# Kernel optimization log

Measured on AMD Instinct MI355X. Metric: run time of the kernel, lower is better.

## Reference

```python
import jax, jax.numpy as jnp
import numpy as np

ODIM = 8192      # output dim (slice target)
MSIZE = 64       # tile size
N_BLOCKS = 1024  # size of shared block bank


def setup_inputs() -> dict:
    key = jax.random.key(0)
    k1, k2, k3, k4 = jax.random.split(key, 4)
    x = jax.random.normal(k1, (256, 8192), dtype=jnp.float32)
    # bank of msize x msize module blocks (scaled like fan-in init)
    blocks = jax.random.normal(k2, (N_BLOCKS, MSIZE, MSIZE), dtype=jnp.float32) * 0.02
    bound = 1.0 / np.sqrt(ODIM).astype(np.float32)
    bias = jax.random.uniform(k3, (ODIM,), dtype=jnp.float32, minval=-bound, maxval=bound)
    # parts: [icount, ocount] indices into the block bank
    parts = jax.random.randint(k4, (128, 128), 0, N_BLOCKS)
    return {"x": x, "blocks": blocks, "bias": bias, "parts": parts}


def reference(x, blocks, bias, parts):
    icount, ocount = parts.shape
    m = blocks.shape[-1]
    # build_mosaic: gather blocks per parts and tile into a dense weight matrix
    fc = blocks[parts]                                   # [ic, oc, m, m]
    fc_mat = fc.transpose(0, 2, 1, 3).reshape(icount * m, ocount * m)
    # idim (8192) is divisible by msize, so pad is identity (rem == 0 branch)
    y = x @ fc_mat                                       # [B, oc*m]
    y = y[..., :ODIM] + bias                             # slice + bias; post = Identity
    return y
```

## Files before the change

### kernel.cpp

```cpp
#include <hip/hip_runtime.h>
#include <stdint.h>

#define BATCH 256
#define IDIM  8192
#define ODIM  8192
#define MS    64
#define IC    128
#define OC    128
#define NB    1024

#define TM 128
#define TN 128
#define KSPLIT 4
#define NIB (IC / KSPLIT)

#define A_BASE(s) ((s) * 8192)
#define B_BASE(s) (16384 + (s) * 8192)

typedef __bf16 bf16x8 __attribute__((ext_vector_type(8)));
typedef float  floatx4 __attribute__((ext_vector_type(4)));

#define WAITCNT_VM(n) ((((n) & 15) | (((n) >> 4) << 14)) | 0x70 | 0xF00)

__device__ __forceinline__ void async_load16(unsigned short* lds_p, const unsigned short* g_p) {
    __builtin_amdgcn_global_load_lds(
        (const __attribute__((address_space(1))) unsigned int*)g_p,
        (__attribute__((address_space(3))) unsigned int*)lds_p,
        16, 0, 0);
}

__device__ __forceinline__ unsigned short f32_to_bf16(float f) {
    unsigned int u = __float_as_uint(f);
    u += 0x7FFFu + ((u >> 16) & 1u);
    return (unsigned short)(u >> 16);
}

#define XCONV_BLKS 1024
#define PT_BLKS 64
__global__ void k_convert(const float* __restrict__ x, const float* __restrict__ blocks,
                          const int* __restrict__ parts,
                          unsigned short* __restrict__ xb, unsigned short* __restrict__ bt,
                          int* __restrict__ pT) {
    __shared__ float tile[MS][MS + 1];
    int b = blockIdx.x;
    if (b < NB) {
        const float4* src4 = (const float4*)(blocks + (size_t)b * MS * MS);
        unsigned short* dst = bt + (size_t)b * MS * MS;
        #pragma unroll
        for (int i = 0; i < 4; ++i) {
            int slot = i * 256 + threadIdx.x;
            int r = slot >> 4, c4 = (slot & 15) * 4;
            float4 v = src4[slot];
            tile[r][c4 + 0] = v.x; tile[r][c4 + 1] = v.y;
            tile[r][c4 + 2] = v.z; tile[r][c4 + 3] = v.w;
        }
        __syncthreads();
        #pragma unroll
        for (int i = 0; i < 2; ++i) {
            int slot = i * 256 + threadIdx.x;
            int c = slot >> 3, o = slot & 7;
            union { unsigned short s[8]; uint4 v; } u;
            #pragma unroll
            for (int j = 0; j < 8; ++j) u.s[j] = f32_to_bf16(tile[o * 8 + j][c]);
            *(uint4*)(dst + c * MS + o * 8) = u.v;
        }
    } else if (b < NB + XCONV_BLKS) {
        int t = (b - NB) * 256 + threadIdx.x;
        const float4* x4 = (const float4*)x;
        float4 a = x4[2 * t], bb = x4[2 * t + 1];
        union { unsigned short s[8]; uint4 v; } u;
        u.s[0] = f32_to_bf16(a.x);  u.s[1] = f32_to_bf16(a.y);
        u.s[2] = f32_to_bf16(a.z);  u.s[3] = f32_to_bf16(a.w);
        u.s[4] = f32_to_bf16(bb.x); u.s[5] = f32_to_bf16(bb.y);
        u.s[6] = f32_to_bf16(bb.z); u.s[7] = f32_to_bf16(bb.w);
        ((uint4*)xb)[t] = u.v;
    } else {
        int t = (b - NB - XCONV_BLKS) * 256 + threadIdx.x;
        int oc = t >> 7, ic = t & 127;
        pT[t] = parts[ic * OC + oc];
    }
}

extern __shared__ unsigned short smem[];

__global__ __launch_bounds__(256, 2)
void k_mosaic_gemm(const unsigned short* __restrict__ xb,
                   const unsigned short* __restrict__ bt,
                   const int* __restrict__ pT,
                   float* __restrict__ partial) {
    const int tid  = threadIdx.x;
    const int lane = tid & 63;
    const int wave = tid >> 6;
    const int wrow = wave >> 1;
    const int wcol = wave & 1;
    const int nt = blockIdx.x;
    const int mt = blockIdx.y;
    const int ks = blockIdx.z;

    const int m0  = mt * TM;
    const int ob0 = nt * 2;
    const int ib0 = ks * NIB;

    const int row  = lane & 15;
    const int quad = lane >> 4;

    int pv0 = pT[ob0 * IC + ib0 + (lane & 31)];
    int pv1 = pT[(ob0 + 1) * IC + ib0 + (lane & 31)];

    int a_off[2][4], b_off[2][4];
    #pragma unroll
    for (int kk = 0; kk < 2; ++kk) {
        int oct = kk * 4 + quad;
        #pragma unroll
        for (int mi = 0; mi < 4; ++mi) {
            int r = wrow * 64 + mi * 16 + row;
            a_off[kk][mi] = r * MS + ((oct ^ (r & 7)) << 3);
        }
        #pragma unroll
        for (int ni = 0; ni < 4; ++ni) {
            int n = wcol * 64 + ni * 16 + row;
            b_off[kk][ni] = n * MS + ((oct ^ (n & 7)) << 3);
        }
    }

    floatx4 acc[4][4];
    #pragma unroll
    for (int mi = 0; mi < 4; ++mi)
        #pragma unroll
        for (int ni = 0; ni < 4; ++ni)
            acc[mi][ni] = (floatx4){0.f, 0.f, 0.f, 0.f};

#define STAGE_A(abase, ibx) do {                                              \
    _Pragma("unroll")                                                         \
    for (int j = 0; j < 4; ++j) {                                             \
        int slot = j * 256 + tid;               \
        int m = slot >> 3;                                                    \
        int oct = (slot & 7) ^ (m & 7);                                       \
        async_load16(smem + (abase) + slot * 8,                               \
                     xb + (size_t)(m0 + m) * IDIM + (ibx) * MS + oct * 8);    \
    } } while (0)

#define STAGE_B(bbase, pa, pb) do {                                           \
    _Pragma("unroll")                                                         \
    for (int j = 0; j < 4; ++j) {                                             \
        int slot = j * 256 + tid;               \
        int n = slot >> 3;                                                    \
        int oct = (slot & 7) ^ (n & 7);                                       \
        int p = (j < 2) ? (pa) : (pb);                                        \
        async_load16(smem + (bbase) + slot * 8,                               \
                     bt + (size_t)p * (MS * MS) + (n & 63) * MS + oct * 8);   \
    } } while (0)

#define COMPUTE(abase, bbase) do {                                            \
    _Pragma("unroll")                                                         \
    for (int kk = 0; kk < 2; ++kk) {                                          \
        bf16x8 af[4], bfr[4];                                                 \
        _Pragma("unroll")                                                     \
        for (int mi = 0; mi < 4; ++mi)                                        \
            af[mi] = *(const bf16x8*)(smem + (abase) + a_off[kk][mi]);        \
        _Pragma("unroll")                                                     \
        for (int ni = 0; ni < 4; ++ni)                                        \
            bfr[ni] = *(const bf16x8*)(smem + (bbase) + b_off[kk][ni]);       \
        _Pragma("unroll")                                                     \
        for (int mi = 0; mi < 4; ++mi)                                        \
            _Pragma("unroll")                                                 \
            for (int ni = 0; ni < 4; ++ni)                                    \
                acc[mi][ni] = __builtin_amdgcn_mfma_f32_16x16x32_bf16(        \
                    af[mi], bfr[ni], acc[mi][ni], 0, 0, 0);                   \
    } } while (0)

#define ROUND(idx, acS, bcS, asS, bsS) do {                                   \
    STAGE_A(A_BASE(asS), ib0 + (idx) + 1);                                    \
    { int q0 = __shfl(pv0, (idx) + 2), q1 = __shfl(pv1, (idx) + 2);           \
      STAGE_B(B_BASE(bsS), q0, q1); }                                         \
    __builtin_amdgcn_sched_barrier(0);                                        \
    __builtin_amdgcn_s_waitcnt(WAITCNT_VM(12));                               \
    __builtin_amdgcn_s_barrier();                                             \
    __builtin_amdgcn_sched_barrier(0);                                        \
    COMPUTE(A_BASE(acS), B_BASE(bcS));                                        \
    __builtin_amdgcn_sched_barrier(0);                                        \
    __builtin_amdgcn_s_barrier();                                             \
    __builtin_amdgcn_sched_barrier(0);                                        \
    } while (0)

    STAGE_A(A_BASE(0), ib0 + 0);
    { int q0 = __shfl(pv0, 0), q1 = __shfl(pv1, 0); STAGE_B(B_BASE(0), q0, q1); }
    { int q0 = __shfl(pv0, 1), q1 = __shfl(pv1, 1); STAGE_B(B_BASE(1), q0, q1); }

    for (int i6 = 0; i6 < 30; i6 += 6) {
        ROUND(i6 + 0, 0, 0, 1, 2);
        ROUND(i6 + 1, 1, 1, 0, 0);
        ROUND(i6 + 2, 0, 2, 1, 1);
        ROUND(i6 + 3, 1, 0, 0, 2);
        ROUND(i6 + 4, 0, 1, 1, 0);
        ROUND(i6 + 5, 1, 2, 0, 1);
    }
    STAGE_A(A_BASE(1), ib0 + NIB - 1);
    __builtin_amdgcn_sched_barrier(0);
    __builtin_amdgcn_s_waitcnt(WAITCNT_VM(8));
    __builtin_amdgcn_s_barrier();
    __builtin_amdgcn_sched_barrier(0);
    COMPUTE(A_BASE(0), B_BASE(0));
    __builtin_amdgcn_sched_barrier(0);
    __builtin_amdgcn_s_barrier();
    __builtin_amdgcn_sched_barrier(0);
    __builtin_amdgcn_s_waitcnt(WAITCNT_VM(0));
    __builtin_amdgcn_s_barrier();
    __builtin_amdgcn_sched_barrier(0);
    COMPUTE(A_BASE(1), B_BASE(1));

    float* out = partial + (size_t)ks * BATCH * ODIM;
    #pragma unroll
    for (int mi = 0; mi < 4; ++mi)
        #pragma unroll
        for (int ni = 0; ni < 4; ++ni)
            #pragma unroll
            for (int r = 0; r < 4; ++r) {
                int rowg = m0 + wrow * 64 + mi * 16 + quad * 4 + r;
                int colg = nt * TN + wcol * 64 + ni * 16 + row;
                out[(size_t)rowg * ODIM + colg] = acc[mi][ni][r];
            }
}

__global__ void k_reduce_bias(const float* __restrict__ partial,
                              const float* __restrict__ bias,
                              float* __restrict__ out) {
    int t = blockIdx.x * 256 + threadIdx.x;
    const float4* b4 = (const float4*)bias;
    float4 c = b4[t & (ODIM / 4 - 1)];
    float4 r = {c.x, c.y, c.z, c.w};
    #pragma unroll
    for (int k = 0; k < KSPLIT; ++k) {
        const float4* p = (const float4*)(partial + (size_t)k * BATCH * ODIM);
        float4 a = p[t];
        r.x += a.x; r.y += a.y; r.z += a.z; r.w += a.w;
    }
    ((float4*)out)[t] = r;
}

extern "C" void kernel_launch(void* const* d_in, const int* in_sizes, int n_in,
                              void* d_out, int out_size, void* d_ws, size_t ws_size,
                              hipStream_t stream) {
    const float* x      = (const float*)d_in[0];
    const float* blocks = (const float*)d_in[1];
    const float* bias   = (const float*)d_in[2];
    const int*   parts  = (const int*)d_in[3];
    float* out = (float*)d_out;

    char* ws = (char*)d_ws;
    unsigned short* xb      = (unsigned short*)ws;
    unsigned short* btb     = (unsigned short*)(ws + (4u << 20));
    int*            pTr     = (int*)(ws + (12u << 20));
    float*          partial = (float*)(ws + (13u << 20));

    static bool attr_set = false;
    if (!attr_set) {
        hipFuncSetAttribute((const void*)k_mosaic_gemm,
                            hipFuncAttributeMaxDynamicSharedMemorySize, 80 * 1024);
        attr_set = true;
    }

    k_convert<<<NB + XCONV_BLKS + PT_BLKS, 256, 0, stream>>>(x, blocks, parts, xb, btb, pTr);
    k_mosaic_gemm<<<dim3(ODIM / TN, BATCH / TM, KSPLIT), 256, 80 * 1024, stream>>>(xb, btb, pTr, partial);
    k_reduce_bias<<<(BATCH * ODIM) / (256 * 4), 256, 0, stream>>>(partial, bias, out);
}
```

Before: 121.4 us.

## Switch GEMM to 256x256 tiles with 512 threads and 8-way K split

Replaces the 128x128-tile, 4-way split-K mosaic GEMM with 256x256 tiles computed by 512-thread blocks over an 8-way K split. The 64-wide K step is double-buffered, with loads and MFMAs interleaved in quarter-tile phases and raised wave priority around the MFMA bursts. The goal is more data reuse per LDS byte and a full one-block-per-CU grid of 256 blocks. In exchange it doubles the split-K partial buffer, so the reduce kernel's memory traffic grows. It also needs 128 KB of LDS, which leaves one block per CU.

Measured after the change: 127.8 us. 1.05x slower.

```diff
diff --git a/kernel.cpp b/kernel.cpp
--- a/kernel.cpp
+++ b/kernel.cpp
@@ -9,13 +9,14 @@
 #define OC    128
 #define NB    1024
 
-#define TM 128
-#define TN 128
-#define KSPLIT 4
-#define NIB (IC / KSPLIT)
-
-#define A_BASE(s) ((s) * 8192)
-#define B_BASE(s) (16384 + (s) * 8192)
+#define BM 256
+#define BN 256
+#define BK 64
+#define KSPLIT 8
+#define KT (IC / KSPLIT)
+
+#define ABUF(s) ((s) * 16384)
+#define BBUF(s) (32768 + (s) * 16384)
 
 typedef __bf16 bf16x8 __attribute__((ext_vector_type(8)));
 typedef float  floatx4 __attribute__((ext_vector_type(4)));
@@ -83,7 +84,7 @@
 
 extern __shared__ unsigned short smem[];
 
-__global__ __launch_bounds__(256, 2)
+__global__ __launch_bounds__(512, 2)
 void k_mosaic_gemm(const unsigned short* __restrict__ xb,
                    const unsigned short* __restrict__ bt,
                    const int* __restrict__ pT,
@@ -91,134 +92,136 @@
     const int tid  = threadIdx.x;
     const int lane = tid & 63;
     const int wave = tid >> 6;
-    const int wrow = wave >> 1;
-    const int wcol = wave & 1;
-    const int nt = blockIdx.x;
-    const int mt = blockIdx.y;
-    const int ks = blockIdx.z;
-
-    const int m0  = mt * TM;
-    const int ob0 = nt * 2;
-    const int ib0 = ks * NIB;
+    const int wrow = wave >> 2;
+    const int wcol = wave & 3;
+    const int ks = blockIdx.x;
+    const int nt = blockIdx.y;
+
+    const int ob0 = nt * 4;
+    const int kb0 = ks * KT;
 
     const int row  = lane & 15;
     const int quad = lane >> 4;
 
-    int pv0 = pT[ob0 * IC + ib0 + (lane & 31)];
-    int pv1 = pT[(ob0 + 1) * IC + ib0 + (lane & 31)];
-
-    int a_off[2][4], b_off[2][4];
+    int pv = pT[(ob0 + quad) * IC + kb0 + row];
+
+    const int swz0 = ((quad)     ^ (row & 7)) << 3;
+    const int swz1 = ((quad + 4) ^ (row & 7)) << 3;
+    const int a_b0 = (wrow * 128 + row) * MS + swz0;
+    const int a_b1 = (wrow * 128 + row) * MS + swz1;
+    const int b_b0 = (wcol * 64 + row) * MS + swz0;
+    const int b_b1 = (wcol * 64 + row) * MS + swz1;
+
+    floatx4 acc[8][4];
     #pragma unroll
-    for (int kk = 0; kk < 2; ++kk) {
-        int oct = kk * 4 + quad;
-        #pragma unroll
-        for (int mi = 0; mi < 4; ++mi) {
-            int r = wrow * 64 + mi * 16 + row;
-            a_off[kk][mi] = r * MS + ((oct ^ (r & 7)) << 3);
-        }
-        #pragma unroll
-        for (int ni = 0; ni < 4; ++ni) {
-            int n = wcol * 64 + ni * 16 + row;
-            b_off[kk][ni] = n * MS + ((oct ^ (n & 7)) << 3);
-        }
-    }
-
-    floatx4 acc[4][4];
-    #pragma unroll
-    for (int mi = 0; mi < 4; ++mi)
+    for (int mi = 0; mi < 8; ++mi)
         #pragma unroll
         for (int ni = 0; ni < 4; ++ni)
             acc[mi][ni] = (floatx4){0.f, 0.f, 0.f, 0.f};
 
-#define STAGE_A(abase, ibx) do {                                              \
+    bf16x8 af[4], bfr[4];
+
+#define STAGE_A(dstS, kb) do {                                                \
     _Pragma("unroll")                                                         \
     for (int j = 0; j < 4; ++j) {                                             \
-        int slot = j * 256 + tid;               \
+        int slot = j * 512 + tid;               \
         int m = slot >> 3;                                                    \
         int oct = (slot & 7) ^ (m & 7);                                       \
-        async_load16(smem + (abase) + slot * 8,                               \
-                     xb + (size_t)(m0 + m) * IDIM + (ibx) * MS + oct * 8);    \
+        async_load16(smem + ABUF(dstS) + slot * 8,                            \
+                     xb + (size_t)m * IDIM + (kb) * MS + oct * 8);            \
     } } while (0)
 
-#define STAGE_B(bbase, pa, pb) do {                                           \
+#define STAGE_B(dstS, t) do {                                                 \
     _Pragma("unroll")                                                         \
     for (int j = 0; j < 4; ++j) {                                             \
-        int slot = j * 256 + tid;               \
+        int q = __shfl(pv, j * 16 + (t));                                     \
+        int slot = j * 512 + tid;                                             \
         int n = slot >> 3;                                                    \
         int oct = (slot & 7) ^ (n & 7);                                       \
-        int p = (j < 2) ? (pa) : (pb);                                        \
-        async_load16(smem + (bbase) + slot * 8,                               \
-                     bt + (size_t)p * (MS * MS) + (n & 63) * MS + oct * 8);   \
+        async_load16(smem + BBUF(dstS) + slot * 8,                            \
+                     bt + (size_t)q * (MS * MS) + (n & 63) * MS + oct * 8);   \
     } } while (0)
 
-#define COMPUTE(abase, bbase) do {                                            \
-    _Pragma("unroll")                                                         \
-    for (int kk = 0; kk < 2; ++kk) {                                          \
-        bf16x8 af[4], bfr[4];                                                 \
-        _Pragma("unroll")                                                     \
-        for (int mi = 0; mi < 4; ++mi)                                        \
-            af[mi] = *(const bf16x8*)(smem + (abase) + a_off[kk][mi]);        \
+#define BARRIER_PIN() do {                                                    \
+    __builtin_amdgcn_sched_barrier(0);                                        \
+    __builtin_amdgcn_s_barrier();                                             \
+    __builtin_amdgcn_sched_barrier(0); } while (0)
+
+#define LOAD_A(S, abase, mh) do {                                             \
+    _Pragma("unroll")                                                         \
+    for (int mi = 0; mi < 4; ++mi)                                            \
+        af[mi] = *(const bf16x8*)(smem + ABUF(S) + (abase) + (mh) * 4096 + mi * 1024); \
+    } while (0)
+
+#define LOAD_B(S, bbase) do {                                                 \
+    _Pragma("unroll")                                                         \
+    for (int ni = 0; ni < 4; ++ni)                                            \
+        bfr[ni] = *(const bf16x8*)(smem + BBUF(S) + (bbase) + ni * 1024);     \
+    } while (0)
+
+#define MFMA16(mh) do {                                                       \
+    __builtin_amdgcn_s_setprio(1);                                            \
+    _Pragma("unroll")                                                         \
+    for (int mi = 0; mi < 4; ++mi)                                            \
         _Pragma("unroll")                                                     \
         for (int ni = 0; ni < 4; ++ni)                                        \
-            bfr[ni] = *(const bf16x8*)(smem + (bbase) + b_off[kk][ni]);       \
-        _Pragma("unroll")                                                     \
-        for (int mi = 0; mi < 4; ++mi)                                        \
-            _Pragma("unroll")                                                 \
-            for (int ni = 0; ni < 4; ++ni)                                    \
-                acc[mi][ni] = __builtin_amdgcn_mfma_f32_16x16x32_bf16(        \
-                    af[mi], bfr[ni], acc[mi][ni], 0, 0, 0);                   \
-    } } while (0)
-
-#define ROUND(idx, acS, bcS, asS, bsS) do {                                   \
-    STAGE_A(A_BASE(asS), ib0 + (idx) + 1);                                    \
-    { int q0 = __shfl(pv0, (idx) + 2), q1 = __shfl(pv1, (idx) + 2);           \
-      STAGE_B(B_BASE(bsS), q0, q1); }                                         \
+            acc[(mh) * 4 + mi][ni] = __builtin_amdgcn_mfma_f32_16x16x32_bf16( \
+                af[mi], bfr[ni], acc[(mh) * 4 + mi][ni], 0, 0, 0);            \
+    __builtin_amdgcn_s_setprio(0); } while (0)
+
+#define TILE(t, curS, nxtS, DO_STAGE) do {                                    \
+                                         \
+    LOAD_A(curS, a_b0, 0); LOAD_B(curS, b_b0);                                \
+    if (DO_STAGE) STAGE_A(nxtS, kb0 + (t) + 1);                               \
+    BARRIER_PIN();                                                            \
+    MFMA16(0);                                                                \
+    BARRIER_PIN();                                                            \
+                                         \
+    LOAD_A(curS, a_b0, 1);                                                    \
+    if (DO_STAGE) STAGE_B(nxtS, (t) + 1);                                     \
+    BARRIER_PIN();                                                            \
+    MFMA16(1);                                                                \
+    BARRIER_PIN();                                                            \
+                                                        \
+    LOAD_A(curS, a_b1, 0); LOAD_B(curS, b_b1);                                \
+    BARRIER_PIN();                                                            \
+    MFMA16(0);                                                                \
+    BARRIER_PIN();                                                            \
+                  \
+    LOAD_A(curS, a_b1, 1);                                                    \
+    BARRIER_PIN();                                                            \
+    MFMA16(1);                                                                \
     __builtin_amdgcn_sched_barrier(0);                                        \
-    __builtin_amdgcn_s_waitcnt(WAITCNT_VM(12));                               \
-    __builtin_amdgcn_s_barrier();                                             \
-    __builtin_amdgcn_sched_barrier(0);                                        \
-    COMPUTE(A_BASE(acS), B_BASE(bcS));                                        \
-    __builtin_amdgcn_sched_barrier(0);                                        \
+    __builtin_amdgcn_s_waitcnt(WAITCNT_VM(0));                                \
     __builtin_amdgcn_s_barrier();                                             \
     __builtin_amdgcn_sched_barrier(0);                                        \
     } while (0)
 
-    STAGE_A(A_BASE(0), ib0 + 0);
-    { int q0 = __shfl(pv0, 0), q1 = __shfl(pv1, 0); STAGE_B(B_BASE(0), q0, q1); }
-    { int q0 = __shfl(pv0, 1), q1 = __shfl(pv1, 1); STAGE_B(B_BASE(1), q0, q1); }
-
-    for (int i6 = 0; i6 < 30; i6 += 6) {
-        ROUND(i6 + 0, 0, 0, 1, 2);
-        ROUND(i6 + 1, 1, 1, 0, 0);
-        ROUND(i6 + 2, 0, 2, 1, 1);
-        ROUND(i6 + 3, 1, 0, 0, 2);
-        ROUND(i6 + 4, 0, 1, 1, 0);
-        ROUND(i6 + 5, 1, 2, 0, 1);
-    }
-    STAGE_A(A_BASE(1), ib0 + NIB - 1);
-    __builtin_amdgcn_sched_barrier(0);
-    __builtin_amdgcn_s_waitcnt(WAITCNT_VM(8));
-    __builtin_amdgcn_s_barrier();
-    __builtin_amdgcn_sched_barrier(0);
-    COMPUTE(A_BASE(0), B_BASE(0));
-    __builtin_amdgcn_sched_barrier(0);
-    __builtin_amdgcn_s_barrier();
+    STAGE_A(0, kb0);
+    STAGE_B(0, 0);
     __builtin_amdgcn_sched_barrier(0);
     __builtin_amdgcn_s_waitcnt(WAITCNT_VM(0));
     __builtin_amdgcn_s_barrier();
     __builtin_amdgcn_sched_barrier(0);
-    COMPUTE(A_BASE(1), B_BASE(1));
-
-    float* out = partial + (size_t)ks * BATCH * ODIM;
+
+    #pragma unroll 1
+    for (int t2 = 0; t2 < 14; t2 += 2) {
+        TILE(t2,     0, 1, 1);
+        TILE(t2 + 1, 1, 0, 1);
+    }
+    TILE(14, 0, 1, 1);
+    TILE(15, 1, 0, 0);
+
+    float* out = partial + (size_t)ks * ((size_t)BATCH * ODIM);
     #pragma unroll
-    for (int mi = 0; mi < 4; ++mi)
+    for (int mi8 = 0; mi8 < 8; ++mi8)
         #pragma unroll
         for (int ni = 0; ni < 4; ++ni)
             #pragma unroll
             for (int r = 0; r < 4; ++r) {
-                int rowg = m0 + wrow * 64 + mi * 16 + quad * 4 + r;
-                int colg = nt * TN + wcol * 64 + ni * 16 + row;
-                out[(size_t)rowg * ODIM + colg] = acc[mi][ni][r];
+                int rowg = wrow * 128 + mi8 * 16 + quad * 4 + r;
+                int colg = nt * BN + wcol * 64 + ni * 16 + row;
+                out[(size_t)rowg * ODIM + colg] = acc[mi8][ni][r];
             }
 }
 
@@ -256,11 +259,11 @@
     static bool attr_set = false;
     if (!attr_set) {
         hipFuncSetAttribute((const void*)k_mosaic_gemm,
-                            hipFuncAttributeMaxDynamicSharedMemorySize, 80 * 1024);
+                            hipFuncAttributeMaxDynamicSharedMemorySize, 128 * 1024);
         attr_set = true;
     }
 
     k_convert<<<NB + XCONV_BLKS + PT_BLKS, 256, 0, stream>>>(x, blocks, parts, xb, btb, pTr);
-    k_mosaic_gemm<<<dim3(ODIM / TN, BATCH / TM, KSPLIT), 256, 80 * 1024, stream>>>(xb, btb, pTr, partial);
+    k_mosaic_gemm<<<dim3(KSPLIT, ODIM / BN), 512, 128 * 1024, stream>>>(xb, btb, pTr, partial);
     k_reduce_bias<<<(BATCH * ODIM) / (256 * 4), 256, 0, stream>>>(partial, bias, out);
 }
```

## Load B blocks straight from global into registers instead of staging in LDS

Applied to the files above, without the earlier changes.

The B operand (the gathered weight block) is no longer copied into a triple-buffered LDS area. Each wave now reads its 64-column slice directly from global memory into registers, and the two k-halves are double-buffered in registers, with the next block prefetched in the middle of each round. This cuts LDS use from 80KB to 32KB and removes the B staging traffic and B LDS reads, which should allow more resident workgroups. In exchange, waves that share a block column load the same B data redundantly through the cache, and more global-load latency sits close to the MFMA issue.

Result: slower. 153.2 us (+26.2%).

```diff
diff --git a/kernel.cpp b/kernel.cpp
--- a/kernel.cpp
+++ b/kernel.cpp
@@ -15,7 +15,6 @@
 #define NIB (IC / KSPLIT)
 
 #define A_BASE(s) ((s) * 8192)
-#define B_BASE(s) (16384 + (s) * 8192)
 
 typedef __bf16 bf16x8 __attribute__((ext_vector_type(8)));
 typedef float  floatx4 __attribute__((ext_vector_type(4)));
@@ -107,7 +106,7 @@
     int pv0 = pT[ob0 * IC + ib0 + (lane & 31)];
     int pv1 = pT[(ob0 + 1) * IC + ib0 + (lane & 31)];
 
-    int a_off[2][4], b_off[2][4];
+    int a_off[2][4];
     #pragma unroll
     for (int kk = 0; kk < 2; ++kk) {
         int oct = kk * 4 + quad;
@@ -116,11 +115,6 @@
             int r = wrow * 64 + mi * 16 + row;
             a_off[kk][mi] = r * MS + ((oct ^ (r & 7)) << 3);
         }
-        #pragma unroll
-        for (int ni = 0; ni < 4; ++ni) {
-            int n = wcol * 64 + ni * 16 + row;
-            b_off[kk][ni] = n * MS + ((oct ^ (n & 7)) << 3);
-        }
     }
 
     floatx4 acc[4][4];
@@ -129,6 +123,8 @@
         #pragma unroll
         for (int ni = 0; ni < 4; ++ni)
             acc[mi][ni] = (floatx4){0.f, 0.f, 0.f, 0.f};
+
+    bf16x8 b0f[4], b1f[4];
 
 #define STAGE_A(abase, ibx) do {                                              \
     _Pragma("unroll")                                                         \
@@ -140,74 +136,54 @@
                      xb + (size_t)(m0 + m) * IDIM + (ibx) * MS + oct * 8);    \
     } } while (0)
 
-#define STAGE_B(bbase, pa, pb) do {                                           \
-    _Pragma("unroll")                                                         \
-    for (int j = 0; j < 4; ++j) {                                             \
-        int slot = j * 256 + tid;               \
-        int n = slot >> 3;                                                    \
-        int oct = (slot & 7) ^ (n & 7);                                       \
-        int p = (j < 2) ? (pa) : (pb);                                        \
-        async_load16(smem + (bbase) + slot * 8,                               \
-                     bt + (size_t)p * (MS * MS) + (n & 63) * MS + oct * 8);   \
-    } } while (0)
-
-#define COMPUTE(abase, bbase) do {                                            \
-    _Pragma("unroll")                                                         \
-    for (int kk = 0; kk < 2; ++kk) {                                          \
-        bf16x8 af[4], bfr[4];                                                 \
-        _Pragma("unroll")                                                     \
-        for (int mi = 0; mi < 4; ++mi)                                        \
-            af[mi] = *(const bf16x8*)(smem + (abase) + a_off[kk][mi]);        \
+#define LOADB(BB, idx, kkh) do {                                              \
+    int sel = wcol ? pv1 : pv0;                                               \
+    int q = __builtin_amdgcn_readfirstlane(__shfl(sel, (idx)));               \
+    const char* bq = (const char*)(bt + (size_t)q * (MS * MS))                \
+                     + row * 128 + quad * 16 + (kkh) * 64;                    \
+    _Pragma("unroll")                                                         \
+    for (int ni = 0; ni < 4; ++ni)                                            \
+        BB[ni] = *(const bf16x8*)(bq + ni * 2048);                            \
+    } while (0)
+
+#define COMPUTE_K(acS, kk, BB) do {                                           \
+    bf16x8 af[4];                                                             \
+    _Pragma("unroll")                                                         \
+    for (int mi = 0; mi < 4; ++mi)                                            \
+        af[mi] = *(const bf16x8*)(smem + A_BASE(acS) + a_off[kk][mi]);        \
+    _Pragma("unroll")                                                         \
+    for (int mi = 0; mi < 4; ++mi)                                            \
         _Pragma("unroll")                                                     \
         for (int ni = 0; ni < 4; ++ni)                                        \
-            bfr[ni] = *(const bf16x8*)(smem + (bbase) + b_off[kk][ni]);       \
-        _Pragma("unroll")                                                     \
-        for (int mi = 0; mi < 4; ++mi)                                        \
-            _Pragma("unroll")                                                 \
-            for (int ni = 0; ni < 4; ++ni)                                    \
-                acc[mi][ni] = __builtin_amdgcn_mfma_f32_16x16x32_bf16(        \
-                    af[mi], bfr[ni], acc[mi][ni], 0, 0, 0);                   \
-    } } while (0)
-
-#define ROUND(idx, acS, bcS, asS, bsS) do {                                   \
-    STAGE_A(A_BASE(asS), ib0 + (idx) + 1);                                    \
-    { int q0 = __shfl(pv0, (idx) + 2), q1 = __shfl(pv1, (idx) + 2);           \
-      STAGE_B(B_BASE(bsS), q0, q1); }                                         \
-    __builtin_amdgcn_sched_barrier(0);                                        \
-    __builtin_amdgcn_s_waitcnt(WAITCNT_VM(12));                               \
+            acc[mi][ni] = __builtin_amdgcn_mfma_f32_16x16x32_bf16(            \
+                af[mi], BB[ni], acc[mi][ni], 0, 0, 0);                        \
+    } while (0)
+
+#define ROUND(idx, acS, asS, STA, MIDB, WN) do {                              \
+    LOADB(b1f, (idx), 1);                                                     \
+    if (STA) STAGE_A(A_BASE(asS), ib0 + (idx) + 1);                           \
+    __builtin_amdgcn_sched_barrier(0);                                        \
+    __builtin_amdgcn_s_waitcnt(WAITCNT_VM(WN));                               \
     __builtin_amdgcn_s_barrier();                                             \
     __builtin_amdgcn_sched_barrier(0);                                        \
-    COMPUTE(A_BASE(acS), B_BASE(bcS));                                        \
+    COMPUTE_K(acS, 0, b0f);                                                   \
+    if (MIDB) LOADB(b0f, (idx) + 1, 0);                                       \
+    COMPUTE_K(acS, 1, b1f);                                                   \
     __builtin_amdgcn_sched_barrier(0);                                        \
     __builtin_amdgcn_s_barrier();                                             \
     __builtin_amdgcn_sched_barrier(0);                                        \
     } while (0)
 
     STAGE_A(A_BASE(0), ib0 + 0);
-    { int q0 = __shfl(pv0, 0), q1 = __shfl(pv1, 0); STAGE_B(B_BASE(0), q0, q1); }
-    { int q0 = __shfl(pv0, 1), q1 = __shfl(pv1, 1); STAGE_B(B_BASE(1), q0, q1); }
-
-    for (int i6 = 0; i6 < 30; i6 += 6) {
-        ROUND(i6 + 0, 0, 0, 1, 2);
-        ROUND(i6 + 1, 1, 1, 0, 0);
-        ROUND(i6 + 2, 0, 2, 1, 1);
-        ROUND(i6 + 3, 1, 0, 0, 2);
-        ROUND(i6 + 4, 0, 1, 1, 0);
-        ROUND(i6 + 5, 1, 2, 0, 1);
-    }
-    STAGE_A(A_BASE(1), ib0 + NIB - 1);
-    __builtin_amdgcn_sched_barrier(0);
-    __builtin_amdgcn_s_waitcnt(WAITCNT_VM(8));
-    __builtin_amdgcn_s_barrier();
-    __builtin_amdgcn_sched_barrier(0);
-    COMPUTE(A_BASE(0), B_BASE(0));
-    __builtin_amdgcn_sched_barrier(0);
-    __builtin_amdgcn_s_barrier();
-    __builtin_amdgcn_sched_barrier(0);
-    __builtin_amdgcn_s_waitcnt(WAITCNT_VM(0));
-    __builtin_amdgcn_s_barrier();
-    __builtin_amdgcn_sched_barrier(0);
-    COMPUTE(A_BASE(1), B_BASE(1));
+    LOADB(b0f, 0, 0);
+
+    #pragma unroll 1
+    for (int r2 = 0; r2 < 30; r2 += 2) {
+        ROUND(r2,     0, 1, 1, 1, 12);
+        ROUND(r2 + 1, 1, 0, 1, 1, 12);
+    }
+    ROUND(30, 0, 1, 1, 1, 12);
+    ROUND(31, 1, 0, 0, 0, 8);
 
     float* out = partial + (size_t)ks * BATCH * ODIM;
     #pragma unroll
@@ -256,11 +232,11 @@
     static bool attr_set = false;
     if (!attr_set) {
         hipFuncSetAttribute((const void*)k_mosaic_gemm,
-                            hipFuncAttributeMaxDynamicSharedMemorySize, 80 * 1024);
+                            hipFuncAttributeMaxDynamicSharedMemorySize, 32 * 1024);
         attr_set = true;
     }
 
     k_convert<<<NB + XCONV_BLKS + PT_BLKS, 256, 0, stream>>>(x, blocks, parts, xb, btb, pTr);
-    k_mosaic_gemm<<<dim3(ODIM / TN, BATCH / TM, KSPLIT), 256, 80 * 1024, stream>>>(xb, btb, pTr, partial);
+    k_mosaic_gemm<<<dim3(ODIM / TN, BATCH / TM, KSPLIT), 256, 32 * 1024, stream>>>(xb, btb, pTr, partial);
     k_reduce_bias<<<(BATCH * ODIM) / (256 * 4), 256, 0, stream>>>(partial, bias, out);
 }
```

## Replace split-K partial buffer and reduce kernel with atomic accumulation into output

Applied to the files above, without the earlier changes.

The output is now initialised with the bias inside the convert kernel. Each split-K slice of the GEMM then atomically adds its tile into the output. This removes the third kernel launch and the partial buffer, along with its write and re-read traffic. In exchange it uses scalar float atomics, four per element, whose summation order is nondeterministic and which may contend or run slower than plain stores.

Result: slower. 128.8 us (+6.1%).

```diff
diff --git a/kernel.cpp b/kernel.cpp
--- a/kernel.cpp
+++ b/kernel.cpp
@@ -37,10 +37,11 @@
 
 #define XCONV_BLKS 1024
 #define PT_BLKS 64
+#define BIAS_BLKS 2048
 __global__ void k_convert(const float* __restrict__ x, const float* __restrict__ blocks,
-                          const int* __restrict__ parts,
+                          const int* __restrict__ parts, const float* __restrict__ bias,
                           unsigned short* __restrict__ xb, unsigned short* __restrict__ bt,
-                          int* __restrict__ pT) {
+                          int* __restrict__ pT, float* __restrict__ out) {
     __shared__ float tile[MS][MS + 1];
     int b = blockIdx.x;
     if (b < NB) {
@@ -74,10 +75,14 @@
         u.s[4] = f32_to_bf16(bb.x); u.s[5] = f32_to_bf16(bb.y);
         u.s[6] = f32_to_bf16(bb.z); u.s[7] = f32_to_bf16(bb.w);
         ((uint4*)xb)[t] = u.v;
-    } else {
+    } else if (b < NB + XCONV_BLKS + PT_BLKS) {
         int t = (b - NB - XCONV_BLKS) * 256 + threadIdx.x;
         int oc = t >> 7, ic = t & 127;
         pT[t] = parts[ic * OC + oc];
+    } else {
+        int t = (b - NB - XCONV_BLKS - PT_BLKS) * 256 + threadIdx.x;
+        const float4* b4 = (const float4*)bias;
+        ((float4*)out)[t] = b4[t & (ODIM / 4 - 1)];
     }
 }
 
@@ -87,7 +92,7 @@
 void k_mosaic_gemm(const unsigned short* __restrict__ xb,
                    const unsigned short* __restrict__ bt,
                    const int* __restrict__ pT,
-                   float* __restrict__ partial) {
+                   float* __restrict__ out) {
     const int tid  = threadIdx.x;
     const int lane = tid & 63;
     const int wave = tid >> 6;
@@ -209,7 +214,6 @@
     __builtin_amdgcn_sched_barrier(0);
     COMPUTE(A_BASE(1), B_BASE(1));
 
-    float* out = partial + (size_t)ks * BATCH * ODIM;
     #pragma unroll
     for (int mi = 0; mi < 4; ++mi)
         #pragma unroll
@@ -218,24 +222,8 @@
             for (int r = 0; r < 4; ++r) {
                 int rowg = m0 + wrow * 64 + mi * 16 + quad * 4 + r;
                 int colg = nt * TN + wcol * 64 + ni * 16 + row;
-                out[(size_t)rowg * ODIM + colg] = acc[mi][ni][r];
+                atomicAdd(&out[(size_t)rowg * ODIM + colg], acc[mi][ni][r]);
             }
-}
-
-__global__ void k_reduce_bias(const float* __restrict__ partial,
-                              const float* __restrict__ bias,
-                              float* __restrict__ out) {
-    int t = blockIdx.x * 256 + threadIdx.x;
-    const float4* b4 = (const float4*)bias;
-    float4 c = b4[t & (ODIM / 4 - 1)];
-    float4 r = {c.x, c.y, c.z, c.w};
-    #pragma unroll
-    for (int k = 0; k < KSPLIT; ++k) {
-        const float4* p = (const float4*)(partial + (size_t)k * BATCH * ODIM);
-        float4 a = p[t];
-        r.x += a.x; r.y += a.y; r.z += a.z; r.w += a.w;
-    }
-    ((float4*)out)[t] = r;
 }
 
 extern "C" void kernel_launch(void* const* d_in, const int* in_sizes, int n_in,
@@ -248,10 +236,9 @@
     float* out = (float*)d_out;
 
     char* ws = (char*)d_ws;
-    unsigned short* xb      = (unsigned short*)ws;
-    unsigned short* btb     = (unsigned short*)(ws + (4u << 20));
-    int*            pTr     = (int*)(ws + (12u << 20));
-    float*          partial = (float*)(ws + (13u << 20));
+    unsigned short* xb  = (unsigned short*)ws;
+    unsigned short* btb = (unsigned short*)(ws + (4u << 20));
+    int*            pTr = (int*)(ws + (12u << 20));
 
     static bool attr_set = false;
     if (!attr_set) {
@@ -260,7 +247,8 @@
         attr_set = true;
     }
 
-    k_convert<<<NB + XCONV_BLKS + PT_BLKS, 256, 0, stream>>>(x, blocks, parts, xb, btb, pTr);
-    k_mosaic_gemm<<<dim3(ODIM / TN, BATCH / TM, KSPLIT), 256, 80 * 1024, stream>>>(xb, btb, pTr, partial);
-    k_reduce_bias<<<(BATCH * ODIM) / (256 * 4), 256, 0, stream>>>(partial, bias, out);
-}
+    k_convert<<<NB + XCONV_BLKS + PT_BLKS + BIAS_BLKS, 256, 0, stream>>>(
+        x, blocks, parts, bias, xb, btb, pTr, out);
+    k_mosaic_gemm<<<dim3(ODIM / TN, BATCH / TM, KSPLIT), 256, 80 * 1024, stream>>>(
+        xb, btb, pTr, out);
+}
```
